# Kernel tuning notes

Measured on AMD Instinct MI355X. Metric: run time of the kernel, lower is better.

## Reference

```python
import jax, jax.numpy as jnp
import numpy as np

R, C, CH, BA = 2048, 1024, 8, 8
EPS = 1e-10


def setup_inputs() -> dict:
    key = jax.random.key(0)
    k1, k2, k3 = jax.random.split(key, 3)
    # kaiming_uniform_ on [R, CH*BA]: fan_in = CH*BA, bound = sqrt(6/fan_in)
    bound = float(np.sqrt(6.0 / (CH * BA)))
    W = jax.random.uniform(k1, (R, CH * BA), jnp.float32, -bound, bound)
    D = (jax.random.uniform(k2, (R, C)) < 0.1).astype(jnp.float32)
    # Gumbel(0,1) noise, replicating the torch quirk: -log(eps - log(u + eps))
    u = jax.random.uniform(k3, (R, CH * BA), jnp.float32)
    g = -jnp.log(EPS - jnp.log(u + EPS))
    return {"W": W, "D": D, "g": g, "i": 100}


def reference(W, D, g, i):
    # temp = 1000 - 999/3999*i is computed in torch but GumbelSoftmax.forward
    # ignores it and always uses temperature=1, so i has no effect on the math.
    P = jax.nn.softmax(W + g, axis=-1).reshape(R, CH, BA)        # [R,CH,BA]
    x = P[:, None, :, :] * D[:, :, None, None]                    # [R,C,CH,BA]

    nnz_ch_ba = jnp.sum(x, axis=(0, 1))                           # [CH,BA]
    max_nnz_ch = jnp.max(nnz_ch_ba, axis=-1)                      # [CH] (torch dim=2 on 2D -> last axis)

    col_ch = 1.0 - jnp.prod(jnp.prod(1.0 - x, axis=0), axis=2)    # [C,CH]
    num_col_ch = jnp.sum(col_ch, axis=0)                          # [CH]
    num_row_ch = jnp.sum(P, axis=(0, 2))                          # [CH]

    col_density_ch = jnp.sum(
        jnp.sum(x, axis=(0, 3)) / num_row_ch / num_col_ch, axis=0)  # [CH]

    tot_ch = max_nnz_ch + num_col_ch + num_row_ch                 # [CH]

    num_row_sel = jnp.sum(
        (jnp.max(P.reshape(R, -1), axis=1) > 0.99).astype(jnp.float32))
    return (P, tot_ch, max_nnz_ch, num_col_ch, num_row_ch,
            nnz_ch_ba, col_density_ch, num_row_sel)
```

## Files before the change

kernel.cpp:

```cpp
#include <hip/hip_runtime.h>
#include <math.h>

#define R 2048
#define C 1024
#define CH 8
#define K 64

#define OFF_P     0
#define OFF_TOT   (R*K)
#define OFF_MAX   (OFF_TOT + 8)
#define OFF_NCOL  (OFF_MAX + 8)
#define OFF_NROW  (OFF_NCOL + 8)
#define OFF_NNZ   (OFF_NROW + 8)
#define OFF_DEN   (OFF_NNZ + 64)
#define OFF_SEL   (OFF_DEN + 8)

#define WS_LQ   0
#define WS_COL  16384
#define WS_NP   24576
#define WS_NR   40960
#define WS_SEL  43008
#define WS_CNT  43264

__global__ __launch_bounds__(512) void k1(
    const float* __restrict__ W, const float* __restrict__ Dm,
    const float* __restrict__ g, float* __restrict__ P,
    float* __restrict__ ws)
{
    const int tid  = threadIdx.x;
    const int lane = tid & 63;
    const int w    = tid >> 6;
    const int row  = blockIdx.x * 8 + w;

    if (tid < 32) ws[WS_COL + blockIdx.x * 32 + tid] = 0.0f;
    if (blockIdx.x == 0 && tid == 32) ((unsigned*)ws)[WS_CNT] = 0u;

    float z = W[row * K + lane] + g[row * K + lane];
    float m = z;
    #pragma unroll
    for (int off = 32; off >= 1; off >>= 1)
        m = fmaxf(m, __shfl_xor(m, off, 64));
    float e = __expf(z - m);
    float s = e;
    #pragma unroll
    for (int off = 32; off >= 1; off >>= 1)
        s += __shfl_xor(s, off, 64);
    float p = e * __builtin_amdgcn_rcpf(s);
    P[row * K + lane] = p;

    const float4* Drow = (const float4*)(Dm + (size_t)row * C);
    float ds = 0.0f;
    #pragma unroll
    for (int j = 0; j < 4; ++j) {
        float4 v = Drow[lane + 64 * j];
        ds += (v.x + v.y) + (v.z + v.w);
    }
    #pragma unroll
    for (int off = 32; off >= 1; off >>= 1)
        ds += __shfl_xor(ds, off, 64);

    float om = 1.0f - p, sc = p;
    #pragma unroll
    for (int off = 1; off <= 4; off <<= 1) {
        om *= __shfl_xor(om, off, 64);
        sc += __shfl_xor(sc, off, 64);
    }
    if ((lane & 7) == 0)
        ws[WS_LQ + row * CH + (lane >> 3)] =
            fmaxf(__builtin_amdgcn_logf(om), -1.0e30f);

    float pm = p;
    #pragma unroll
    for (int off = 32; off >= 1; off >>= 1)
        pm = fmaxf(pm, __shfl_xor(pm, off, 64));

    __shared__ float rn[8][64];
    __shared__ float rp[8][8];
    __shared__ float rsel[8];
    rn[w][lane] = p * ds;
    if ((lane & 7) == 0) rp[w][lane >> 3] = sc;
    if (lane == 0) rsel[w] = (pm > 0.99f) ? 1.0f : 0.0f;
    __syncthreads();

    if (tid < 64) {
        float v = rn[0][tid] + rn[1][tid] + rn[2][tid] + rn[3][tid]
                + rn[4][tid] + rn[5][tid] + rn[6][tid] + rn[7][tid];
        ws[WS_NP + blockIdx.x * 64 + tid] = v;
    }
    if (tid < 8) {
        float v = 0.0f;
        #pragma unroll
        for (int ww = 0; ww < 8; ++ww) v += rp[ww][tid];
        ws[WS_NR + blockIdx.x * 8 + tid] = v;
    }
    if (tid == 0) {
        float v = 0.0f;
        #pragma unroll
        for (int ww = 0; ww < 8; ++ww) v += rsel[ww];
        ws[WS_SEL + blockIdx.x] = v;
    }
}

__global__ __launch_bounds__(512) void k2(
    const float* __restrict__ Dm, float* __restrict__ ws,
    float* __restrict__ out)
{
    const int tid  = threadIdx.x;
    const int ct   = blockIdx.x & 3;
    const int rc   = blockIdx.x >> 2;
    const int c    = tid & 255;
    const int col  = ct * 256 + c;
    const int half = tid >> 8;

    const int r0 = __builtin_amdgcn_readfirstlane(rc * 32 + half * 16);

    float l[8] = {0,0,0,0,0,0,0,0};
    #pragma unroll
    for (int i = 0; i < 16; ++i) {
        const int r = r0 + i;
        const float d = Dm[(size_t)r * C + col];
        const float* lr = ws + WS_LQ + r * CH;
        #pragma unroll
        for (int j = 0; j < 8; ++j) l[j] += d * lr[j];
    }

    __shared__ float comb[8][256];
    if (half) {
        #pragma unroll
        for (int j = 0; j < 8; ++j) comb[j][c] = l[j];
    }
    __syncthreads();
    if (!half) {
        float* ca = ws + WS_COL;
        const int st = rc & 7;
        #pragma unroll
        for (int jj = 0; jj < 8; ++jj) {
            const int j = (jj + st) & 7;
            atomicAdd(&ca[j * 1024 + col], l[j] + comb[j][c]);
        }
    }
    __syncthreads();

    __shared__ int amLast;
    if (tid == 0) {
        unsigned old = __hip_atomic_fetch_add(
            (unsigned*)ws + WS_CNT, 1u,
            __ATOMIC_ACQ_REL, __HIP_MEMORY_SCOPE_AGENT);
        amLast = (old == 255u);
    }
    __syncthreads();
    if (!amLast) return;

    const int fl = tid & 63;
    const int fw = tid >> 6;

    __shared__ float nc8[8];
    __shared__ float npr[8][64];
    __shared__ float nrr[8][8];
    __shared__ float selr[64];

    {
        float ncl = 0.0f;
        #pragma unroll
        for (int j = 0; j < 16; ++j) {
            float sv = ws[WS_COL + fw * 1024 + j * 64 + fl];
            ncl += 1.0f - __builtin_amdgcn_exp2f(sv);
        }
        #pragma unroll
        for (int off = 32; off >= 1; off >>= 1)
            ncl += __shfl_xor(ncl, off, 64);
        if (fl == 0) nc8[fw] = ncl;
    }
    {
        float v = 0.0f;
        #pragma unroll
        for (int b = 0; b < 32; ++b)
            v += ws[WS_NP + (fw * 32 + b) * 64 + fl];
        npr[fw][fl] = v;
    }
    if (tid < 64) {
        const int ch2 = tid & 7, grp = tid >> 3;
        float v = 0.0f;
        #pragma unroll
        for (int b = 0; b < 32; ++b)
            v += ws[WS_NR + (grp * 32 + b) * CH + ch2];
        nrr[grp][ch2] = v;
        float sv = 0.0f;
        #pragma unroll
        for (int j = 0; j < 4; ++j)
            sv += ws[WS_SEL + j * 64 + tid];
        selr[tid] = sv;
    }
    __syncthreads();

    if (tid < 64) {
        float nnzv = 0.0f;
        #pragma unroll
        for (int g2 = 0; g2 < 8; ++g2) nnzv += npr[g2][tid];
        out[OFF_NNZ + tid] = nnzv;

        float sum = nnzv, mx = nnzv;
        #pragma unroll
        for (int off = 1; off <= 4; off <<= 1) {
            sum += __shfl_xor(sum, off, 64);
            mx = fmaxf(mx, __shfl_xor(mx, off, 64));
        }
        float sv = selr[tid];
        #pragma unroll
        for (int off = 32; off >= 1; off >>= 1)
            sv += __shfl_xor(sv, off, 64);
        if (tid == 0) out[OFF_SEL] = sv;

        if ((tid & 7) == 0) {
            const int ch = tid >> 3;
            float nr = 0.0f;
            #pragma unroll
            for (int g2 = 0; g2 < 8; ++g2) nr += nrr[g2][ch];
            const float nc = nc8[ch];
            out[OFF_TOT  + ch] = mx + nc + nr;
            out[OFF_MAX  + ch] = mx;
            out[OFF_NCOL + ch] = nc;
            out[OFF_NROW + ch] = nr;
            out[OFF_DEN  + ch] = sum / nr / nc;
        }
    }
}

extern "C" void kernel_launch(void* const* d_in, const int* in_sizes, int n_in,
                              void* d_out, int out_size, void* d_ws, size_t ws_size,
                              hipStream_t stream) {
    const float* W = (const float*)d_in[0];
    const float* D = (const float*)d_in[1];
    const float* g = (const float*)d_in[2];
    float* out = (float*)d_out;
    float* ws  = (float*)d_ws;

    k1<<<256, 512, 0, stream>>>(W, D, g, out, ws);
    k2<<<256, 512, 0, stream>>>(D, ws, out);
}
```

Before: 78.58 us.

## Replace column atomics with per-chunk partials and a separate reduction kernel

k2 no longer accumulates column log-products with float atomics into a shared buffer. Each row chunk now writes its partial sums to its own slot in a 2MB workspace. A new kernel k3 reduces those partials per channel and column group, computes the column counts, and runs the last-block final reduction. This removes atomic contention and the zeroing pass, but adds an extra kernel launch and more workspace memory traffic.

```diff
diff --git a/kernel.cpp b/kernel.cpp
--- a/kernel.cpp
+++ b/kernel.cpp
@@ -16,11 +16,12 @@
 #define OFF_SEL   (OFF_DEN + 8)
 
 #define WS_LQ   0
-#define WS_COL  16384
 #define WS_NP   24576
 #define WS_NR   40960
 #define WS_SEL  43008
 #define WS_CNT  43264
+#define WS_P2   43328
+#define WS_NC   (WS_P2 + 64*8*1024)
 
 __global__ __launch_bounds__(512) void k1(
     const float* __restrict__ W, const float* __restrict__ Dm,
@@ -32,8 +33,7 @@
     const int w    = tid >> 6;
     const int row  = blockIdx.x * 8 + w;
 
-    if (tid < 32) ws[WS_COL + blockIdx.x * 32 + tid] = 0.0f;
-    if (blockIdx.x == 0 && tid == 32) ((unsigned*)ws)[WS_CNT] = 0u;
+    if (blockIdx.x == 0 && tid == 0) ((unsigned*)ws)[WS_CNT] = 0u;
 
     float z = W[row * K + lane] + g[row * K + lane];
     float m = z;
@@ -102,8 +102,7 @@
 }
 
 __global__ __launch_bounds__(512) void k2(
-    const float* __restrict__ Dm, float* __restrict__ ws,
-    float* __restrict__ out)
+    const float* __restrict__ Dm, float* __restrict__ ws)
 {
     const int tid  = threadIdx.x;
     const int ct   = blockIdx.x & 3;
@@ -131,18 +130,46 @@
     }
     __syncthreads();
     if (!half) {
-        float* ca = ws + WS_COL;
-        const int st = rc & 7;
-        #pragma unroll
-        for (int jj = 0; jj < 8; ++jj) {
-            const int j = (jj + st) & 7;
-            atomicAdd(&ca[j * 1024 + col], l[j] + comb[j][c]);
-        }
+        float* o = ws + WS_P2 + rc * 8192;
+        #pragma unroll
+        for (int j = 0; j < 8; ++j)
+            o[j * 1024 + col] = l[j] + comb[j][c];
+    }
+}
+
+__global__ __launch_bounds__(512) void k3(float* __restrict__ ws,
+                                          float* __restrict__ out)
+{
+    const int tid = threadIdx.x;
+    const int ch  = blockIdx.x >> 5;
+    const int cg  = blockIdx.x & 31;
+    const int cl  = tid & 31;
+    const int rh  = tid >> 5;
+
+    float acc = 0.0f;
+    #pragma unroll
+    for (int j = 0; j < 4; ++j)
+        acc += ws[WS_P2 + ((rh * 4 + j) * 8 + ch) * 1024 + cg * 32 + cl];
+
+    __shared__ float part[32][17];
+    part[cl][rh] = acc;
+    __syncthreads();
+
+    if (tid < 32) {
+        float ca = 0.0f;
+        #pragma unroll
+        for (int h = 0; h < 16; ++h) ca += part[tid][h];
+        float ncl = 1.0f - __builtin_amdgcn_exp2f(ca);
+        #pragma unroll
+        for (int off = 16; off >= 1; off >>= 1)
+            ncl += __shfl_xor(ncl, off, 64);
+        if (tid == 0) ws[WS_NC + blockIdx.x] = ncl;
     }
     __syncthreads();
 
     __shared__ int amLast;
     if (tid == 0) {
+        __threadfence();
         unsigned old = __hip_atomic_fetch_add(
             (unsigned*)ws + WS_CNT, 1u,
             __ATOMIC_ACQ_REL, __HIP_MEMORY_SCOPE_AGENT);
@@ -160,16 +187,11 @@
     __shared__ float selr[64];
 
     {
-        float ncl = 0.0f;
-        #pragma unroll
-        for (int j = 0; j < 16; ++j) {
-            float sv = ws[WS_COL + fw * 1024 + j * 64 + fl];
-            ncl += 1.0f - __builtin_amdgcn_exp2f(sv);
-        }
+        float v = (fl < 32) ? ws[WS_NC + fw * 32 + fl] : 0.0f;
         #pragma unroll
         for (int off = 32; off >= 1; off >>= 1)
-            ncl += __shfl_xor(ncl, off, 64);
-        if (fl == 0) nc8[fw] = ncl;
+            v += __shfl_xor(v, off, 64);
+        if (fl == 0) nc8[fw] = v;
     }
     {
         float v = 0.0f;
@@ -212,16 +234,16 @@
         if (tid == 0) out[OFF_SEL] = sv;
 
         if ((tid & 7) == 0) {
-            const int ch = tid >> 3;
+            const int chf = tid >> 3;
             float nr = 0.0f;
             #pragma unroll
-            for (int g2 = 0; g2 < 8; ++g2) nr += nrr[g2][ch];
-            const float nc = nc8[ch];
-            out[OFF_TOT  + ch] = mx + nc + nr;
-            out[OFF_MAX  + ch] = mx;
-            out[OFF_NCOL + ch] = nc;
-            out[OFF_NROW + ch] = nr;
-            out[OFF_DEN  + ch] = sum / nr / nc;
+            for (int g2 = 0; g2 < 8; ++g2) nr += nrr[g2][chf];
+            const float nc = nc8[chf];
+            out[OFF_TOT  + chf] = mx + nc + nr;
+            out[OFF_MAX  + chf] = mx;
+            out[OFF_NCOL + chf] = nc;
+            out[OFF_NROW + chf] = nr;
+            out[OFF_DEN  + chf] = sum / nr / nc;
         }
     }
 }
@@ -236,5 +258,6 @@
     float* ws  = (float*)d_ws;
 
     k1<<<256, 512, 0, stream>>>(W, D, g, out, ws);
-    k2<<<256, 512, 0, stream>>>(D, ws, out);
-}
+    k2<<<256, 512, 0, stream>>>(D, ws);
+    k3<<<256, 512, 0, stream>>>(ws, out);
+}
```

Result: slower. 83.88 us (+6.7%).

## Fuse softmax and column-product kernels with per-chunk spin-wait flags

Applied to the files above, without the earlier changes.

Merges the two kernels into one 256-block kernel where each block first computes its 8 rows of softmax stats, then signals a per-32-row chunk counter and spin-waits until the 4 blocks producing its chunk are done before doing the column log-product accumulation. Workspace zeroing moves into a tiny separate kernel launched first. The intent is to replace the global kernel boundary with fine-grained dependencies so phases overlap. It relies on all 256 blocks being co-resident to avoid deadlock, and it adds atomic and spin costs.

```diff
diff --git a/kernel.cpp b/kernel.cpp
--- a/kernel.cpp
+++ b/kernel.cpp
@@ -17,134 +17,149 @@
 
 #define WS_LQ   0
 #define WS_COL  16384
-#define WS_NP   24576
-#define WS_NR   40960
-#define WS_SEL  43008
-#define WS_CNT  43264
-
-__global__ __launch_bounds__(512) void k1(
+#define WS_CNT  24576
+#define WS_NP   24704
+#define WS_NR   41088
+#define WS_SEL  43136
+
+__global__ __launch_bounds__(1024) void k0(float* __restrict__ ws)
+{
+    const int idx = blockIdx.x * 1024 + threadIdx.x;
+    if (idx < 8192 + 66) ws[WS_COL + idx] = 0.0f;
+}
+
+__global__ __launch_bounds__(512) void kmain(
     const float* __restrict__ W, const float* __restrict__ Dm,
-    const float* __restrict__ g, float* __restrict__ P,
+    const float* __restrict__ g, float* __restrict__ out,
     float* __restrict__ ws)
 {
     const int tid  = threadIdx.x;
     const int lane = tid & 63;
     const int w    = tid >> 6;
-    const int row  = blockIdx.x * 8 + w;
-
-    if (tid < 32) ws[WS_COL + blockIdx.x * 32 + tid] = 0.0f;
-    if (blockIdx.x == 0 && tid == 32) ((unsigned*)ws)[WS_CNT] = 0u;
-
-    float z = W[row * K + lane] + g[row * K + lane];
-    float m = z;
-    #pragma unroll
-    for (int off = 32; off >= 1; off >>= 1)
-        m = fmaxf(m, __shfl_xor(m, off, 64));
-    float e = __expf(z - m);
-    float s = e;
-    #pragma unroll
-    for (int off = 32; off >= 1; off >>= 1)
-        s += __shfl_xor(s, off, 64);
-    float p = e * __builtin_amdgcn_rcpf(s);
-    P[row * K + lane] = p;
-
-    const float4* Drow = (const float4*)(Dm + (size_t)row * C);
-    float ds = 0.0f;
-    #pragma unroll
-    for (int j = 0; j < 4; ++j) {
-        float4 v = Drow[lane + 64 * j];
-        ds += (v.x + v.y) + (v.z + v.w);
-    }
-    #pragma unroll
-    for (int off = 32; off >= 1; off >>= 1)
-        ds += __shfl_xor(ds, off, 64);
-
-    float om = 1.0f - p, sc = p;
-    #pragma unroll
-    for (int off = 1; off <= 4; off <<= 1) {
-        om *= __shfl_xor(om, off, 64);
-        sc += __shfl_xor(sc, off, 64);
-    }
-    if ((lane & 7) == 0)
-        ws[WS_LQ + row * CH + (lane >> 3)] =
-            fmaxf(__builtin_amdgcn_logf(om), -1.0e30f);
-
-    float pm = p;
-    #pragma unroll
-    for (int off = 32; off >= 1; off >>= 1)
-        pm = fmaxf(pm, __shfl_xor(pm, off, 64));
-
-    __shared__ float rn[8][64];
-    __shared__ float rp[8][8];
-    __shared__ float rsel[8];
-    rn[w][lane] = p * ds;
-    if ((lane & 7) == 0) rp[w][lane >> 3] = sc;
-    if (lane == 0) rsel[w] = (pm > 0.99f) ? 1.0f : 0.0f;
-    __syncthreads();
-
-    if (tid < 64) {
-        float v = rn[0][tid] + rn[1][tid] + rn[2][tid] + rn[3][tid]
-                + rn[4][tid] + rn[5][tid] + rn[6][tid] + rn[7][tid];
-        ws[WS_NP + blockIdx.x * 64 + tid] = v;
-    }
-    if (tid < 8) {
-        float v = 0.0f;
-        #pragma unroll
-        for (int ww = 0; ww < 8; ++ww) v += rp[ww][tid];
-        ws[WS_NR + blockIdx.x * 8 + tid] = v;
-    }
-    if (tid == 0) {
-        float v = 0.0f;
-        #pragma unroll
-        for (int ww = 0; ww < 8; ++ww) v += rsel[ww];
-        ws[WS_SEL + blockIdx.x] = v;
-    }
-}
-
-__global__ __launch_bounds__(512) void k2(
-    const float* __restrict__ Dm, float* __restrict__ ws,
-    float* __restrict__ out)
-{
-    const int tid  = threadIdx.x;
-    const int ct   = blockIdx.x & 3;
-    const int rc   = blockIdx.x >> 2;
-    const int c    = tid & 255;
-    const int col  = ct * 256 + c;
-    const int half = tid >> 8;
-
-    const int r0 = __builtin_amdgcn_readfirstlane(rc * 32 + half * 16);
-
-    float l[8] = {0,0,0,0,0,0,0,0};
-    #pragma unroll
-    for (int i = 0; i < 16; ++i) {
-        const int r = r0 + i;
-        const float d = Dm[(size_t)r * C + col];
-        const float* lr = ws + WS_LQ + r * CH;
-        #pragma unroll
-        for (int j = 0; j < 8; ++j) l[j] += d * lr[j];
-    }
-
-    __shared__ float comb[8][256];
-    if (half) {
-        #pragma unroll
-        for (int j = 0; j < 8; ++j) comb[j][c] = l[j];
-    }
-    __syncthreads();
-    if (!half) {
-        float* ca = ws + WS_COL;
-        const int st = rc & 7;
-        #pragma unroll
-        for (int jj = 0; jj < 8; ++jj) {
-            const int j = (jj + st) & 7;
-            atomicAdd(&ca[j * 1024 + col], l[j] + comb[j][c]);
-        }
-    }
-    __syncthreads();
+    const int b    = blockIdx.x;
+    unsigned* cnt  = (unsigned*)ws + WS_CNT;
+
+    {
+        const int row = b * 8 + w;
+
+        float z = W[row * K + lane] + g[row * K + lane];
+        float m = z;
+        #pragma unroll
+        for (int off = 32; off >= 1; off >>= 1)
+            m = fmaxf(m, __shfl_xor(m, off, 64));
+        float e = __expf(z - m);
+        float s = e;
+        #pragma unroll
+        for (int off = 32; off >= 1; off >>= 1)
+            s += __shfl_xor(s, off, 64);
+        float p = e * __builtin_amdgcn_rcpf(s);
+        out[OFF_P + row * K + lane] = p;
+
+        const float4* Drow = (const float4*)(Dm + (size_t)row * C);
+        float ds = 0.0f;
+        #pragma unroll
+        for (int j = 0; j < 4; ++j) {
+            float4 v = Drow[lane + 64 * j];
+            ds += (v.x + v.y) + (v.z + v.w);
+        }
+        #pragma unroll
+        for (int off = 32; off >= 1; off >>= 1)
+            ds += __shfl_xor(ds, off, 64);
+
+        float om = 1.0f - p, sc = p;
+        #pragma unroll
+        for (int off = 1; off <= 4; off <<= 1) {
+            om *= __shfl_xor(om, off, 64);
+            sc += __shfl_xor(sc, off, 64);
+        }
+        if ((lane & 7) == 0)
+            ws[WS_LQ + row * CH + (lane >> 3)] =
+                fmaxf(__builtin_amdgcn_logf(om), -1.0e30f);
+
+        float pm = p;
+        #pragma unroll
+        for (int off = 32; off >= 1; off >>= 1)
+            pm = fmaxf(pm, __shfl_xor(pm, off, 64));
+
+        __shared__ float rn[8][64];
+        __shared__ float rp[8][8];
+        __shared__ float rsel[8];
+        rn[w][lane] = p * ds;
+        if ((lane & 7) == 0) rp[w][lane >> 3] = sc;
+        if (lane == 0) rsel[w] = (pm > 0.99f) ? 1.0f : 0.0f;
+        __syncthreads();
+
+        if (tid == 0)
+            __hip_atomic_fetch_add(cnt + (b >> 2), 1u,
+                __ATOMIC_RELEASE, __HIP_MEMORY_SCOPE_AGENT);
+
+        if (tid < 64) {
+            float v = rn[0][tid] + rn[1][tid] + rn[2][tid] + rn[3][tid]
+                    + rn[4][tid] + rn[5][tid] + rn[6][tid] + rn[7][tid];
+            ws[WS_NP + b * 64 + tid] = v;
+        }
+        if (tid < 8) {
+            float v = 0.0f;
+            #pragma unroll
+            for (int ww = 0; ww < 8; ++ww) v += rp[ww][tid];
+            ws[WS_NR + b * 8 + tid] = v;
+        }
+        if (tid == 0) {
+            float v = 0.0f;
+            #pragma unroll
+            for (int ww = 0; ww < 8; ++ww) v += rsel[ww];
+            ws[WS_SEL + b] = v;
+        }
+    }
+
+    {
+        const int ct   = b & 3;
+        const int rc   = b >> 2;
+        const int c    = tid & 255;
+        const int col  = ct * 256 + c;
+        const int half = tid >> 8;
+
+        if (tid == 0) {
+            while (__hip_atomic_load(cnt + rc,
+                       __ATOMIC_ACQUIRE, __HIP_MEMORY_SCOPE_AGENT) < 4u)
+                __builtin_amdgcn_s_sleep(1);
+        }
+        __syncthreads();
+
+        const int r0 = __builtin_amdgcn_readfirstlane(rc * 32 + half * 16);
+
+        float l[8] = {0,0,0,0,0,0,0,0};
+        #pragma unroll
+        for (int i = 0; i < 16; ++i) {
+            const int r = r0 + i;
+            const float d = Dm[(size_t)r * C + col];
+            const float* lr = ws + WS_LQ + r * CH;
+            #pragma unroll
+            for (int j = 0; j < 8; ++j) l[j] += d * lr[j];
+        }
+
+        __shared__ float comb[8][256];
+        if (half) {
+            #pragma unroll
+            for (int j = 0; j < 8; ++j) comb[j][c] = l[j];
+        }
+        __syncthreads();
+        if (!half) {
+            float* ca = ws + WS_COL;
+            const int st = rc & 7;
+            #pragma unroll
+            for (int jj = 0; jj < 8; ++jj) {
+                const int j = (jj + st) & 7;
+                atomicAdd(&ca[j * 1024 + col], l[j] + comb[j][c]);
+            }
+        }
+        __syncthreads();
+    }
 
     __shared__ int amLast;
     if (tid == 0) {
-        unsigned old = __hip_atomic_fetch_add(
-            (unsigned*)ws + WS_CNT, 1u,
+        __threadfence();
+        unsigned old = __hip_atomic_fetch_add(cnt + 64, 1u,
             __ATOMIC_ACQ_REL, __HIP_MEMORY_SCOPE_AGENT);
         amLast = (old == 255u);
     }
@@ -174,16 +189,16 @@
     {
         float v = 0.0f;
         #pragma unroll
-        for (int b = 0; b < 32; ++b)
-            v += ws[WS_NP + (fw * 32 + b) * 64 + fl];
+        for (int bb = 0; bb < 32; ++bb)
+            v += ws[WS_NP + (fw * 32 + bb) * 64 + fl];
         npr[fw][fl] = v;
     }
     if (tid < 64) {
         const int ch2 = tid & 7, grp = tid >> 3;
         float v = 0.0f;
         #pragma unroll
-        for (int b = 0; b < 32; ++b)
-            v += ws[WS_NR + (grp * 32 + b) * CH + ch2];
+        for (int bb = 0; bb < 32; ++bb)
+            v += ws[WS_NR + (grp * 32 + bb) * CH + ch2];
         nrr[grp][ch2] = v;
         float sv = 0.0f;
         #pragma unroll
@@ -212,16 +227,16 @@
         if (tid == 0) out[OFF_SEL] = sv;
 
         if ((tid & 7) == 0) {
-            const int ch = tid >> 3;
+            const int chf = tid >> 3;
             float nr = 0.0f;
             #pragma unroll
-            for (int g2 = 0; g2 < 8; ++g2) nr += nrr[g2][ch];
-            const float nc = nc8[ch];
-            out[OFF_TOT  + ch] = mx + nc + nr;
-            out[OFF_MAX  + ch] = mx;
-            out[OFF_NCOL + ch] = nc;
-            out[OFF_NROW + ch] = nr;
-            out[OFF_DEN  + ch] = sum / nr / nc;
+            for (int g2 = 0; g2 < 8; ++g2) nr += nrr[g2][chf];
+            const float nc = nc8[chf];
+            out[OFF_TOT  + chf] = mx + nc + nr;
+            out[OFF_MAX  + chf] = mx;
+            out[OFF_NCOL + chf] = nc;
+            out[OFF_NROW + chf] = nr;
+            out[OFF_DEN  + chf] = sum / nr / nc;
         }
     }
 }
@@ -235,6 +250,6 @@
     float* out = (float*)d_out;
     float* ws  = (float*)d_ws;
 
-    k1<<<256, 512, 0, stream>>>(W, D, g, out, ws);
-    k2<<<256, 512, 0, stream>>>(D, ws, out);
+    k0<<<9, 1024, 0, stream>>>(ws);
+    kmain<<<256, 512, 0, stream>>>(W, D, g, out, ws);
 }
```

Result: slower. 88.57 us (+12.7%).
